# Kernel optimization log

Hardware: AMD Instinct MI355X
Metric: run time of the kernel (lower is better)

## Reference

```python
import jax, jax.numpy as jnp
import numpy as np

K = 16  # neighbors


def _knn_indices(coords, k):
    # coords: (B, 3, N) -> indices (B, N, k) of k nearest points (incl. self)
    sq = jnp.sum(coords * coords, axis=1)                      # (B, N)
    d2 = sq[:, :, None] + sq[:, None, :] - 2.0 * jnp.einsum('bcn,bcm->bnm', coords, coords)
    _, idx = jax.lax.top_k(-d2, k)                             # smallest distances
    return idx


def _gather(points, idx):
    # points: (B, C, N), idx: (B, N, k) -> (B, C, N, k)
    return jax.vmap(lambda p, i: p[:, i])(points, idx)


def setup_inputs() -> dict:
    key = jax.random.key(0)
    ks = jax.random.split(key, 8)
    B, N, C_IN, C_OUT = 4, 8192, 64, 64
    s = 0.05
    return {
        'features': jax.random.normal(ks[0], (B, C_IN, N), dtype=jnp.float32),
        'coords': jax.random.normal(ks[1], (B, 3, N), dtype=jnp.float32),
        'w_lin': jax.random.normal(ks[2], (3 * C_OUT, C_IN), dtype=jnp.float32) * s,
        'w_theta1': jax.random.normal(ks[3], (C_OUT, 3), dtype=jnp.float32) * s,
        'w_theta2': jax.random.normal(ks[4], (C_OUT, C_OUT), dtype=jnp.float32) * s,
        'w_gamma1': jax.random.normal(ks[5], (C_OUT, C_OUT), dtype=jnp.float32) * s,
        'w_gamma2': jax.random.normal(ks[6], (C_OUT, C_OUT), dtype=jnp.float32) * s,
    }


def reference(features, coords, w_lin, w_theta1, w_theta2, w_gamma1, w_gamma2):
    # KNN (int indices, non-differentiable)
    idx = _knn_indices(coords, K)                              # (B, N, k)

    knn_coords = _gather(coords, idx)                          # (B, 3, N, k)
    rel = coords[:, :, :, None] - knn_coords                   # localize * -1
    delta = jnp.einsum('oc,bcnk->bonk', w_theta1, rel)
    delta = jax.nn.relu(jnp.einsum('oc,bcnk->bonk', w_theta2, delta))  # (B, Co, N, k)

    # input linear -> phi, psi, alpha
    feat3 = jnp.einsum('oc,bcn->bon', w_lin, features)         # (B, 3*Co, N)
    phi, psi, alpha = jnp.split(feat3, 3, axis=1)

    psi_g = _gather(psi, idx)                                  # (B, Co, N, k)
    inputs_gamma = phi[:, :, :, None] - psi_g + delta          # localize*-1 + delta
    g = jnp.einsum('oc,bcnk->bonk', w_gamma1, inputs_gamma)
    g = jax.nn.relu(jnp.einsum('oc,bcnk->bonk', w_gamma2, g))
    rho = jax.nn.softmax(g, axis=-1)                           # softmax over k

    alpha_g = _gather(alpha, idx) + delta                      # (B, Co, N, k)
    return jnp.sum(rho * alpha_g, axis=-1)                     # (B, Co, N)
```

## Files before the change

### kernel.cpp

```cpp
#include <hip/hip_runtime.h>
#include <cstdint>


#define NPT 8192
typedef unsigned long long u64;
typedef unsigned int u32;
typedef unsigned short u16;
typedef __attribute__((ext_vector_type(8))) short bf8_t;
typedef __attribute__((ext_vector_type(4))) float f32x4;

__device__ __forceinline__ u16 f2bf(float x) {
  return (u16)((__float_as_uint(x) + 0x8000u) >> 16);
}
__device__ __forceinline__ u32 pkbf(float lo, float hi) {
  return (u32)f2bf(lo) | ((u32)f2bf(hi) << 16);
}
__device__ __forceinline__ float bf2f(u16 v) {
  return __uint_as_float((u32)v << 16);
}
__device__ __forceinline__ u32 med3u(u32 a, u32 b, u32 c) {
  u32 d;
  asm("v_med3_u32 %0, %1, %2, %3" : "=v"(d) : "v"(a), "v"(b), "v"(c));
  return d;
}
__device__ __forceinline__ u32 umin2(u32 a, u32 b) { return a < b ? a : b; }
__device__ __forceinline__ u32 umax2(u32 a, u32 b) { return a > b ? a : b; }
__device__ __forceinline__ float rfl_f(float x) {
  return __uint_as_float((u32)__builtin_amdgcn_readfirstlane((int)__float_as_uint(x)));
}
__device__ __forceinline__ u32 wave_min_u32(u32 v) {
  u32 t;
  t = (u32)__builtin_amdgcn_update_dpp((int)v, (int)v, 0x111, 0xF, 0xF, false); v = umin2(v, t);
  t = (u32)__builtin_amdgcn_update_dpp((int)v, (int)v, 0x112, 0xF, 0xF, false); v = umin2(v, t);
  t = (u32)__builtin_amdgcn_update_dpp((int)v, (int)v, 0x114, 0xF, 0xF, false); v = umin2(v, t);
  t = (u32)__builtin_amdgcn_update_dpp((int)v, (int)v, 0x118, 0xF, 0xF, false); v = umin2(v, t);
  t = (u32)__builtin_amdgcn_update_dpp((int)v, (int)v, 0x142, 0xF, 0xF, false); v = umin2(v, t);
  t = (u32)__builtin_amdgcn_update_dpp((int)v, (int)v, 0x143, 0xF, 0xF, false); v = umin2(v, t);
  return (u32)__builtin_amdgcn_readlane((int)v, 63);
}
__device__ __forceinline__ void ins8(u32* a, u32 key) {
  a[7] = med3u(key, a[6], a[7]);
  a[6] = med3u(key, a[5], a[6]);
  a[5] = med3u(key, a[4], a[5]);
  a[4] = med3u(key, a[3], a[4]);
  a[3] = med3u(key, a[2], a[3]);
  a[2] = med3u(key, a[1], a[2]);
  a[1] = med3u(key, a[0], a[1]);
  a[0] = umin2(a[0], key);
}

__global__ __launch_bounds__(256) void fold1_k(
    const float* __restrict__ wg1, const float* __restrict__ wg2,
    const float* __restrict__ wt1, const float* __restrict__ wt2,
    float* __restrict__ G, float* __restrict__ Mrow, float* __restrict__ McT) {
  int t = blockIdx.x * 256 + threadIdx.x;
  if (t < 4096) {
    int o = t >> 6, c = t & 63;
    float acc = 0.f;
    for (int cp = 0; cp < 64; ++cp) acc = fmaf(wg2[o * 64 + cp], wg1[cp * 64 + c], acc);
    G[o * 64 + c] = acc;
  } else if (t < 4096 + 192) {
    int i = t - 4096;
    int o = i / 3, j = i - o * 3;
    float acc = 0.f;
    for (int c = 0; c < 64; ++c) acc = fmaf(wt2[o * 64 + c], wt1[c * 3 + j], acc);
    Mrow[o * 3 + j] = acc;
    McT[j * 64 + o] = acc;
  }
}

__global__ __launch_bounds__(256) void fold2_k(
    const float* __restrict__ G, const float* __restrict__ wl,
    u16* __restrict__ GF, u16* __restrict__ WF) {
  int t = blockIdx.x * 256 + threadIdx.x;
  if (t < 12288) {
    int o = t >> 6, c = t & 63;
    float acc = 0.f;
    if (o < 64) {
      for (int cp = 0; cp < 64; ++cp) acc = fmaf(G[o * 64 + cp], wl[cp * 64 + c], acc);
    } else if (o < 128) {
      for (int cp = 0; cp < 64; ++cp) acc = fmaf(G[(o - 64) * 64 + cp], wl[(64 + cp) * 64 + c], acc);
    } else {
      acc = wl[o * 64 + c];
    }
    int ot = o >> 4, m = o & 15;
    int kh = c >> 5, q = (c >> 3) & 3, j = c & 7;
    WF[(((ot * 2 + kh) * 64) + (q * 16 + m)) * 8 + j] = f2bf(acc);
  } else {
    int i = t - 12288;
    int o = i >> 6, c = i & 63;
    int ot = o >> 4, m = o & 15;
    int kh = c >> 5, q = (c >> 3) & 3, j = c & 7;
    GF[(((ot * 2 + kh) * 64) + (q * 16 + m)) * 8 + j] = f2bf(G[o * 64 + c]);
  }
}

__global__ __launch_bounds__(256) void pack_k(const float* __restrict__ coords,
                                              float4* __restrict__ pack) {
  int g = blockIdx.x * 256 + threadIdx.x;
  int b = g >> 13, n = g & (NPT - 1);
  const float* c = coords + (size_t)b * 3 * NPT;
  float x = c[n], y = c[NPT + n], z = c[2 * NPT + n];
  float sq = __fadd_rn(__fadd_rn(__fmul_rn(x, x), __fmul_rn(y, y)), __fmul_rn(z, z));
  pack[g] = make_float4(x, y, z, sq);
}

#define NB 1024
#define XMIN -5.0f
#define BW 0.009765625f
#define INVBW 102.4f
#define NQ 32768

__global__ __launch_bounds__(1024) void zero_k(u32* __restrict__ cnt) {
  cnt[blockIdx.x * 1024 + threadIdx.x] = 0;
}

__global__ __launch_bounds__(256) void cnt_k(const float4* __restrict__ pack,
                                             u32* __restrict__ cnt) {
  int g = blockIdx.x * 256 + threadIdx.x;
  int b = g >> 13;
  float x = pack[g].x;
  int bi = (int)floorf((x - XMIN) * INVBW);
  bi = bi < 0 ? 0 : (bi > NB - 1 ? NB - 1 : bi);
  atomicAdd(&cnt[b * NB + bi], 1u);
}

__global__ __launch_bounds__(1024) void scan_k(const u32* __restrict__ cnt,
                                               u32* __restrict__ cursor) {
  __shared__ u32 S[NB];
  int b = blockIdx.x, t = threadIdx.x;
  u32 own = cnt[b * NB + t];
  S[t] = own;
  __syncthreads();
  for (int off = 1; off < NB; off <<= 1) {
    u32 v = (t >= off) ? S[t - off] : 0u;
    __syncthreads();
    S[t] += v;
    __syncthreads();
  }
  cursor[b * NB + t] = S[t] - own;
}

__global__ __launch_bounds__(256) void scat_k(const float4* __restrict__ pack,
                                              u32* __restrict__ cursor,
                                              float4* __restrict__ spack,
                                              int* __restrict__ sidx,
                                              float* __restrict__ xedge) {
  int g = blockIdx.x * 256 + threadIdx.x;
  int b = g >> 13, n = g & (NPT - 1);
  float4 p = pack[g];
  int bi = (int)floorf((p.x - XMIN) * INVBW);
  bi = bi < 0 ? 0 : (bi > NB - 1 ? NB - 1 : bi);
  u32 pos = atomicAdd(&cursor[b * NB + bi], 1u);
  size_t o = (size_t)b * NPT + pos;
  spack[o] = p;
  sidx[o] = n;
  xedge[o] = fmaf((float)bi, BW, XMIN);
}

#define QW 4
__global__ __launch_bounds__(256) void knn_k(const float4* __restrict__ spack,
                                             const float* __restrict__ xedge,
                                             u32* __restrict__ part24) {
  int tid = threadIdx.x;
  int wid = tid >> 6, lane = tid & 63;
  int gw = blockIdx.x * 4 + wid;
  int b = gw >> 11;
  int gb = gw & 2047;
  int gbs = (gb & 31) * 64 + (gb >> 5);
  int c0 = gbs * QW;
  const float4* sp = spack + (size_t)b * NPT;
  const float* xe = xedge + (size_t)b * NPT;
  float qx[QW], qy[QW], qz[QW], qs[QW];
#pragma unroll
  for (int j = 0; j < QW; ++j) {
    float4 qv = sp[c0 + j];
    qx[j] = rfl_f(qv.x); qy[j] = rfl_f(qv.y);
    qz[j] = rfl_f(qv.z); qs[j] = rfl_f(qv.w);
  }
  float qxmax = fmaxf(fmaxf(qx[0], qx[1]), fmaxf(qx[2], qx[3]));
  float qxmin = fminf(fminf(qx[0], qx[1]), fminf(qx[2], qx[3]));
  u32 arr[QW][8];
#pragma unroll
  for (int j = 0; j < QW; ++j)
#pragma unroll
    for (int s = 0; s < 8; ++s) arr[j][s] = 0xFFFFFFFFu;
  int R = c0, L = c0;
  bool ra = true, la = (c0 > 0);
#pragma unroll 1
  while (ra || la) {
    if (ra) {
      int cand = R + lane;
      bool ok = cand < NPT;
      int cc = ok ? cand : NPT - 1;
      float4 p = sp[cc];
      u32 kbad = ok ? 0u : 0xFFFFFFFFu;
#pragma unroll
      for (int j = 0; j < QW; ++j) {
        float dot = fmaf(qz[j], p.z, fmaf(qy[j], p.y, qx[j] * p.x));
        float d2 = fmaxf(fmaf(-2.f, dot, qs[j] + p.w), 0.f);
        u32 key = ((__float_as_uint(d2) & 0xFFFFE000u) | (u32)cc) | kbad;
        ins8(arr[j], key);
      }
      R += 64;
      if (R >= NPT) ra = false;
    }
    if (la) {
      int base = L - 64;
      int cand = base + lane;
      bool ok = cand >= 0;
      int cc = ok ? cand : 0;
      float4 p = sp[cc];
      u32 kbad = ok ? 0u : 0xFFFFFFFFu;
#pragma unroll
      for (int j = 0; j < QW; ++j) {
        float dot = fmaf(qz[j], p.z, fmaf(qy[j], p.y, qx[j] * p.x));
        float d2 = fmaxf(fmaf(-2.f, dot, qs[j] + p.w), 0.f);
        u32 key = ((__float_as_uint(d2) & 0xFFFFE000u) | (u32)cc) | kbad;
        ins8(arr[j], key);
      }
      L = base;
      if (L <= 0) la = false;
    }
    u32 pm = umax2(umax2(arr[0][7], arr[1][7]), umax2(arr[2][7], arr[3][7]));
    u32 sw = (u32)__builtin_amdgcn_update_dpp((int)pm, (int)pm, 0xB1, 0xF, 0xF, false);
    u32 B = wave_min_u32(umax2(pm, sw));
    if (B < 0xFF000000u) {
      float tf = __uint_as_float((B & 0xFFFFE000u) + 0x20000u);
      if (ra) {
        float dxr = (xe[R] - 1e-3f) - qxmax;
        if (dxr > 0.f && dxr * dxr > tf) ra = false;
      }
      if (la) {
        float dxl = qxmin - (xe[L - 1] + (BW + 1e-3f));
        if (dxl > 0.f && dxl * dxl > tf) la = false;
      }
    }
  }
#pragma unroll
  for (int j = 0; j < QW; ++j) {
    u32 mg = 0xFFFFFFFFu;
#pragma unroll 1
    for (int r = 0; r < 24; ++r) {
      u32 m = wave_min_u32(arr[j][0]);
      if (lane == r) mg = m;
      if (arr[j][0] == m) {
        arr[j][0] = arr[j][1]; arr[j][1] = arr[j][2];
        arr[j][2] = arr[j][3]; arr[j][3] = arr[j][4];
        arr[j][4] = arr[j][5]; arr[j][5] = arr[j][6];
        arr[j][6] = arr[j][7]; arr[j][7] = 0xFFFFFFFFu;
      }
    }
    if (lane < 24) part24[((size_t)b * NPT + c0 + j) * 24 + lane] = mg;
  }
}

__global__ __launch_bounds__(64) void refine_k(const float4* __restrict__ spack,
                                               const int* __restrict__ sidx,
                                               const u32* __restrict__ part24,
                                               int* __restrict__ idxk) {
  int gs = blockIdx.x * 64 + threadIdx.x;
  int b = gs >> 13;
  const float4* sp = spack + (size_t)b * NPT;
  const int* si = sidx + (size_t)b * NPT;
  int qid = sidx[gs];
  float4 q = spack[gs];
  float qx = q.x, qy = q.y, qz = q.z, qs = q.w;
  float bd[16];
  int bi[16];
#pragma unroll
  for (int j = 0; j < 16; ++j) { bd[j] = 1e30f; bi[j] = 0x7FFFFFFF; }
#pragma unroll 4
  for (int j = 0; j < 24; ++j) {
    int ms = (int)(part24[(size_t)gs * 24 + j] & 0x1FFFu);
    float4 pm = sp[ms];
    int ki = si[ms];
    float dot = __fadd_rn(__fadd_rn(__fmul_rn(qx, pm.x), __fmul_rn(qy, pm.y)),
                          __fmul_rn(qz, pm.z));
    float kd = __fsub_rn(__fadd_rn(qs, pm.w), __fmul_rn(2.0f, dot));
    if (kd < bd[15] || (kd == bd[15] && ki < bi[15])) {
#pragma unroll
      for (int qq = 0; qq < 16; ++qq) {
        bool cs = (kd < bd[qq]) || (kd == bd[qq] && ki < bi[qq]);
        float td = bd[qq];
        int ti = bi[qq];
        bd[qq] = cs ? kd : td;
        bi[qq] = cs ? ki : ti;
        kd = cs ? td : kd;
        ki = cs ? ti : ki;
      }
    }
  }
#pragma unroll
  for (int j = 0; j < 16; ++j) idxk[(size_t)(((size_t)b * NPT + qid)) * 16 + j] = bi[j];
}

__global__ __launch_bounds__(256) void feat_k(const float* __restrict__ features,
                                              const u16* __restrict__ WF,
                                              float* __restrict__ featA,
                                              u16* __restrict__ featB) {
  int tid = threadIdx.x;
  int w = tid >> 6, l = tid & 63;
  int quad = l >> 4, col = l & 15;
  int P = blockIdx.x * 64 + w * 16 + col;
  int b = P >> 13, n = P & (NPT - 1);
  const float* fb = features + (size_t)b * 64 * NPT + n;
  const bf8_t* wfr = (const bf8_t*)WF;
  bf8_t Bf[2];
#pragma unroll
  for (int kh = 0; kh < 2; ++kh) {
    union { u32 wv[4]; bf8_t v; } ub;
#pragma unroll
    for (int j2 = 0; j2 < 4; ++j2) {
      float lo = fb[(size_t)(kh * 32 + quad * 8 + j2 * 2) * NPT];
      float hi = fb[(size_t)(kh * 32 + quad * 8 + j2 * 2 + 1) * NPT];
      ub.wv[j2] = pkbf(lo, hi);
    }
    Bf[kh] = ub.v;
  }
#pragma unroll
  for (int ot = 0; ot < 12; ++ot) {
    bf8_t A0 = wfr[(ot * 2 + 0) * 64 + l];
    bf8_t A1 = wfr[(ot * 2 + 1) * 64 + l];
    f32x4 acc = {0.f, 0.f, 0.f, 0.f};
    acc = __builtin_amdgcn_mfma_f32_16x16x32_bf16(A0, Bf[0], acc, 0, 0, 0);
    acc = __builtin_amdgcn_mfma_f32_16x16x32_bf16(A1, Bf[1], acc, 0, 0, 0);
    int gr = ot * 16 + quad * 4;
    if (ot < 4) {
      *(float4*)(featA + (size_t)P * 64 + gr) = make_float4(acc[0], acc[1], acc[2], acc[3]);
    } else {
      uint2 wv2 = make_uint2(pkbf(acc[0], acc[1]), pkbf(acc[2], acc[3]));
      *(uint2*)(featB + (size_t)P * 128 + (gr - 64)) = wv2;
    }
  }
}

#define SROW 68
__global__ __launch_bounds__(64) void attn_k(
    const float4* __restrict__ pack, const int* __restrict__ idxk,
    const float* __restrict__ featA, const u16* __restrict__ featB,
    const u16* __restrict__ GF, const float* __restrict__ Mrow,
    const float* __restrict__ McT, float* __restrict__ out) {
  __shared__ u16 S16[64 * SROW];
  int l = threadIdx.x;
  int quad = l >> 4, col = l & 15;
  int Pb = blockIdx.x * 4;
  int b = Pb >> 13;
  int nb0 = Pb & (NPT - 1);
  const float4* pkb = pack + (size_t)b * NPT;
  int idxv = idxk[(size_t)Pb * 16 + l];
  int mve[4];
#pragma unroll
  for (int t = 0; t < 4; ++t) mve[t] = __shfl(idxv, t * 16 + col);
  float relx[4], rely[4], relz[4];
#pragma unroll
  for (int t = 0; t < 4; ++t) {
    float4 own = pkb[nb0 + t];
    float4 nbr = pkb[mve[t]];
    relx[t] = own.x - nbr.x; rely[t] = own.y - nbr.y; relz[t] = own.z - nbr.z;
  }
  bf8_t Bf[4][2];
#pragma unroll
  for (int kh = 0; kh < 2; ++kh) {
    const float* mr = Mrow + (kh * 32 + quad * 8) * 3;
    float m_[24];
#pragma unroll
    for (int i6 = 0; i6 < 6; ++i6) {
      float4 v = *(const float4*)(mr + i6 * 4);
      m_[i6 * 4] = v.x; m_[i6 * 4 + 1] = v.y; m_[i6 * 4 + 2] = v.z; m_[i6 * 4 + 3] = v.w;
    }
#pragma unroll
    for (int t = 0; t < 4; ++t) {
      float u_[8];
#pragma unroll
      for (int j = 0; j < 8; ++j)
        u_[j] = fmaxf(fmaf(m_[j * 3 + 2], relz[t],
                           fmaf(m_[j * 3 + 1], rely[t], m_[j * 3] * relx[t])), 0.f);
      union { u32 w[4]; bf8_t v; } ub;
#pragma unroll
      for (int j2 = 0; j2 < 4; ++j2) ub.w[j2] = pkbf(u_[j2 * 2], u_[j2 * 2 + 1]);
      Bf[t][kh] = ub.v;
    }
  }
  const bf8_t* gfr = (const bf8_t*)GF;
#pragma unroll
  for (int ot = 0; ot < 4; ++ot) {
    bf8_t A0 = gfr[(ot * 2 + 0) * 64 + l];
    bf8_t A1 = gfr[(ot * 2 + 1) * 64 + l];
#pragma unroll
    for (int pt = 0; pt < 4; ++pt) {
      f32x4 acc = {0.f, 0.f, 0.f, 0.f};
      acc = __builtin_amdgcn_mfma_f32_16x16x32_bf16(A0, Bf[pt][0], acc, 0, 0, 0);
      acc = __builtin_amdgcn_mfma_f32_16x16x32_bf16(A1, Bf[pt][1], acc, 0, 0, 0);
      const float* phn = featA + (size_t)(Pb + pt) * 64 + ot * 16 + quad * 4;
      float4 ph = *(const float4*)phn;
      uint2 psw = *(const uint2*)(featB + ((size_t)b * NPT + mve[pt]) * 128 + ot * 16 + quad * 4);
      float g0 = fmaxf(acc[0] + ph.x - bf2f((u16)(psw.x & 0xFFFF)), 0.f);
      float g1 = fmaxf(acc[1] + ph.y - bf2f((u16)(psw.x >> 16)), 0.f);
      float g2 = fmaxf(acc[2] + ph.z - bf2f((u16)(psw.y & 0xFFFF)), 0.f);
      float g3 = fmaxf(acc[3] + ph.w - bf2f((u16)(psw.y >> 16)), 0.f);
      uint2 wv = make_uint2(pkbf(g0, g1), pkbf(g2, g3));
      *(uint2*)&S16[(pt * 16 + col) * SROW + ot * 16 + quad * 4] = wv;
    }
  }
  __syncthreads();
  float mc0 = McT[l], mc1 = McT[64 + l], mc2 = McT[128 + l];
  float accv[4];
#pragma unroll 1
  for (int pj = 0; pj < 4; ++pj) {
    float4 ownq = pkb[nb0 + pj];
    float gvv[16];
    float mx = -1e30f;
#pragma unroll
    for (int r = 0; r < 16; ++r) {
      gvv[r] = bf2f(S16[(pj * 16 + r) * SROW + l]);
      mx = fmaxf(mx, gvv[r]);
    }
    float s = 0.f;
#pragma unroll
    for (int r = 0; r < 16; ++r) {
      float e = __expf(gvv[r] - mx);
      gvv[r] = e;
      s += e;
    }
    float inv = 1.0f / s;
    float acc = 0.f;
#pragma unroll
    for (int r = 0; r < 16; ++r) {
      int si = __builtin_amdgcn_readlane(idxv, pj * 16 + r);
      float dl = fmaxf(fmaf(mc2, ownq.z - pkb[si].z,
                            fmaf(mc1, ownq.y - pkb[si].y, mc0 * (ownq.x - pkb[si].x))), 0.f);
      float al = bf2f(featB[((size_t)b * NPT + si) * 128 + 64 + l]);
      acc = fmaf(gvv[r] * inv, al + dl, acc);
    }
    accv[pj] = acc;
  }
  *(float4*)(out + ((size_t)b * 64 + l) * NPT + nb0) =
      make_float4(accv[0], accv[1], accv[2], accv[3]);
}

extern "C" void kernel_launch(void* const* d_in, const int* in_sizes, int n_in,
                              void* d_out, int out_size, void* d_ws, size_t ws_size,
                              hipStream_t stream) {
  const float* features = (const float*)d_in[0];
  const float* coords = (const float*)d_in[1];
  const float* w_lin = (const float*)d_in[2];
  const float* w_t1 = (const float*)d_in[3];
  const float* w_t2 = (const float*)d_in[4];
  const float* w_g1 = (const float*)d_in[5];
  const float* w_g2 = (const float*)d_in[6];
  float* out = (float*)d_out;
  char* ws = (char*)d_ws;
  float4* pack = (float4*)ws;
  float* G = (float*)(ws + 524288);
  float* Mrow = (float*)(ws + 540672);
  float* McT = (float*)(ws + 541440);
  int* idxk = (int*)(ws + 591360);
  float* featA = (float*)(ws + 2688512);
  u16* featB = (u16*)(ws + 11077120);
  u32* part24 = (u32*)(ws + 2688512);
  float4* spack = (float4*)(ws + 11077120);
  int* sidx = (int*)(ws + 11601408);
  float* xedge = (float*)(ws + 11732480);
  u32* cnt = (u32*)(ws + 11863552);
  u32* cursor = (u32*)(ws + 11879936);
  u16* GF = (u16*)(ws + 19465728);
  u16* WF = (u16*)(ws + 19473920);

  fold1_k<<<17, 256, 0, stream>>>(w_g1, w_g2, w_t1, w_t2, G, Mrow, McT);
  fold2_k<<<64, 256, 0, stream>>>(G, w_lin, GF, WF);
  pack_k<<<128, 256, 0, stream>>>(coords, pack);
  zero_k<<<4, 1024, 0, stream>>>(cnt);
  cnt_k<<<128, 256, 0, stream>>>(pack, cnt);
  scan_k<<<4, 1024, 0, stream>>>(cnt, cursor);
  scat_k<<<128, 256, 0, stream>>>(pack, cursor, spack, sidx, xedge);
  knn_k<<<2048, 256, 0, stream>>>(spack, xedge, part24);
  refine_k<<<512, 64, 0, stream>>>(spack, sidx, part24, idxk);
  feat_k<<<512, 256, 0, stream>>>(features, WF, featA, featB);
  attn_k<<<8192, 64, 0, stream>>>(pack, idxk, featA, featB, GF, Mrow, McT, out);
}
```

Measured before the change: 315.8 us.

## Seed KNN pruning bound from warmup scan with exact 16th-neighbor distance

The KNN kernel now scans a fixed warmup window of 8 chunks in each direction. It then computes a tight pruning bound from the true 16th-smallest candidate per query, extracted by wave-wide pops. That bound stays fixed while the scan expands, which removes the per-iteration wave reduction, but a stale bound may scan more chunks than the old adaptive one. Query-to-wave mapping also changes from a strided swizzle to contiguous sorted-order assignment.

Result: faster. 306.4 us (-3.0%).

```diff
diff --git a/kernel.cpp b/kernel.cpp
--- a/kernel.cpp
+++ b/kernel.cpp
@@ -47,6 +47,20 @@
   a[2] = med3u(key, a[1], a[2]);
   a[1] = med3u(key, a[0], a[1]);
   a[0] = umin2(a[0], key);
+}
+__device__ __forceinline__ u32 pop16(const u32* a) {
+  u32 t0 = a[0], t1 = a[1], t2 = a[2], t3 = a[3];
+  u32 t4 = a[4], t5 = a[5], t6 = a[6], t7 = a[7];
+  u32 m = 0xFFFFFFFFu;
+#pragma unroll 1
+  for (int r = 0; r < 16; ++r) {
+    m = wave_min_u32(t0);
+    if (t0 == m) {
+      t0 = t1; t1 = t2; t2 = t3; t3 = t4; t4 = t5; t5 = t6; t6 = t7;
+      t7 = 0xFFFFFFFFu;
+    }
+  }
+  return m;
 }
 
 __global__ __launch_bounds__(256) void fold1_k(
@@ -164,11 +178,8 @@
                                              u32* __restrict__ part24) {
   int tid = threadIdx.x;
   int wid = tid >> 6, lane = tid & 63;
-  int gw = blockIdx.x * 4 + wid;
-  int b = gw >> 11;
-  int gb = gw & 2047;
-  int gbs = (gb & 31) * 64 + (gb >> 5);
-  int c0 = gbs * QW;
+  int q0 = blockIdx.x * (4 * QW) + wid * QW;
+  int b = q0 >> 13, c0 = q0 & (NPT - 1);
   const float4* sp = spack + (size_t)b * NPT;
   const float* xe = xedge + (size_t)b * NPT;
   float qx[QW], qy[QW], qz[QW], qs[QW];
@@ -185,57 +196,47 @@
   for (int j = 0; j < QW; ++j)
 #pragma unroll
     for (int s = 0; s < 8; ++s) arr[j][s] = 0xFFFFFFFFu;
+
+  auto scan_at = [&](int base) {
+    int cand = base + lane;
+    bool ok = (cand >= 0) && (cand < NPT);
+    int cc = ok ? cand : (cand < 0 ? 0 : NPT - 1);
+    float4 p = sp[cc];
+    u32 kbad = ok ? 0u : 0xFFFFFFFFu;
+#pragma unroll
+    for (int j = 0; j < QW; ++j) {
+      float dot = fmaf(qz[j], p.z, fmaf(qy[j], p.y, qx[j] * p.x));
+      float d2 = fmaxf(fmaf(-2.f, dot, qs[j] + p.w), 0.f);
+      u32 key = ((__float_as_uint(d2) & 0xFFFFE000u) | (u32)cc) | kbad;
+      ins8(arr[j], key);
+    }
+  };
+
   int R = c0, L = c0;
-  bool ra = true, la = (c0 > 0);
+#pragma unroll 1
+  for (int it = 0; it < 8; ++it) {
+    if (R < NPT) { scan_at(R); R += 64; }
+    if (L > 0)   { L -= 64; scan_at(L); }
+  }
+  u32 B = 0;
+#pragma unroll 1
+  for (int j = 0; j < QW; ++j) B = umax2(B, pop16(arr[j]));
+  float tf = __uint_as_float((B & 0xFFFFE000u) + 0x20000u);
+  bool useB = (B < 0xFF000000u);
+  bool ra = (R < NPT), la = (L > 0);
 #pragma unroll 1
   while (ra || la) {
-    if (ra) {
-      int cand = R + lane;
-      bool ok = cand < NPT;
-      int cc = ok ? cand : NPT - 1;
-      float4 p = sp[cc];
-      u32 kbad = ok ? 0u : 0xFFFFFFFFu;
-#pragma unroll
-      for (int j = 0; j < QW; ++j) {
-        float dot = fmaf(qz[j], p.z, fmaf(qy[j], p.y, qx[j] * p.x));
-        float d2 = fmaxf(fmaf(-2.f, dot, qs[j] + p.w), 0.f);
-        u32 key = ((__float_as_uint(d2) & 0xFFFFE000u) | (u32)cc) | kbad;
-        ins8(arr[j], key);
-      }
-      R += 64;
-      if (R >= NPT) ra = false;
-    }
-    if (la) {
-      int base = L - 64;
-      int cand = base + lane;
-      bool ok = cand >= 0;
-      int cc = ok ? cand : 0;
-      float4 p = sp[cc];
-      u32 kbad = ok ? 0u : 0xFFFFFFFFu;
-#pragma unroll
-      for (int j = 0; j < QW; ++j) {
-        float dot = fmaf(qz[j], p.z, fmaf(qy[j], p.y, qx[j] * p.x));
-        float d2 = fmaxf(fmaf(-2.f, dot, qs[j] + p.w), 0.f);
-        u32 key = ((__float_as_uint(d2) & 0xFFFFE000u) | (u32)cc) | kbad;
-        ins8(arr[j], key);
-      }
-      L = base;
-      if (L <= 0) la = false;
-    }
-    u32 pm = umax2(umax2(arr[0][7], arr[1][7]), umax2(arr[2][7], arr[3][7]));
-    u32 sw = (u32)__builtin_amdgcn_update_dpp((int)pm, (int)pm, 0xB1, 0xF, 0xF, false);
-    u32 B = wave_min_u32(umax2(pm, sw));
-    if (B < 0xFF000000u) {
-      float tf = __uint_as_float((B & 0xFFFFE000u) + 0x20000u);
-      if (ra) {
-        float dxr = (xe[R] - 1e-3f) - qxmax;
-        if (dxr > 0.f && dxr * dxr > tf) ra = false;
-      }
-      if (la) {
-        float dxl = qxmin - (xe[L - 1] + (BW + 1e-3f));
-        if (dxl > 0.f && dxl * dxl > tf) la = false;
-      }
-    }
+    if (ra && useB) {
+      float dxr = (xe[R] - 1e-3f) - qxmax;
+      if (dxr > 0.f && dxr * dxr > tf) ra = false;
+    }
+    if (la && useB) {
+      float dxl = qxmin - (xe[L - 1] + (BW + 1e-3f));
+      if (dxl > 0.f && dxl * dxl > tf) la = false;
+    }
+    if (!(ra || la)) break;
+    if (ra) { scan_at(R); R += 64; ra = (R < NPT); }
+    if (la) { L -= 64; scan_at(L); la = (L > 0); }
   }
 #pragma unroll
   for (int j = 0; j < QW; ++j) {
```
